# Optimization experiments

Hardware: AMD Instinct MI355X
Metric: run time of the kernel (lower is better)

Reference implementation:

```python
import jax, jax.numpy as jnp
import numpy as np

KH = KW = 5          # deformable kernel (matches offset_channels = 2*5*5)
PAD = 2              # (5-1)//2
DG = 4               # deformable groups


def conv3d(x, w, padding, bias=None):
    # x: [N,C,D,H,W], w: [O,I,kd,kh,kw]
    out = jax.lax.conv_general_dilated(
        x, w, window_strides=(1, 1, 1), padding=padding,
        dimension_numbers=('NCDHW', 'OIDHW', 'NCDHW'))
    if bias is not None:
        out = out + bias[None, :, None, None, None]
    return out


def deform_conv2d(x, offset, weight, pad=PAD, dg=DG):
    """torchvision/mmcv-style deformable conv, stride 1, groups=1, no bias.
    x: [N,C,H,W]; offset: [N, dg*2*K, H, W] ordered (group, k, (dy,dx));
    weight: [Cout, C, KH, KW]."""
    N, C, H, W = x.shape
    K = KH * KW
    off = offset.reshape(N, dg, K, 2, H, W)
    ky, kx = jnp.meshgrid(jnp.arange(KH), jnp.arange(KW), indexing='ij')
    ky = ky.reshape(K).astype(x.dtype)
    kx = kx.reshape(K).astype(x.dtype)
    # absolute sampling positions: [N,dg,K,H,W]
    base_y = ky[:, None, None] - pad + jnp.arange(H, dtype=x.dtype)[None, :, None]
    base_x = kx[:, None, None] - pad + jnp.arange(W, dtype=x.dtype)[None, None, :]
    sy = base_y[None, None] + off[:, :, :, 0]
    sx = base_x[None, None] + off[:, :, :, 1]
    y0 = jnp.floor(sy)
    x0 = jnp.floor(sx)
    wy = sy - y0
    wx = sx - x0
    y0i = y0.astype(jnp.int32)
    x0i = x0.astype(jnp.int32)
    Cg = C // dg
    xg = x.reshape(N, dg, Cg, H * W)

    def gather(yi, xi):
        valid = (yi >= 0) & (yi < H) & (xi >= 0) & (xi < W)
        yc = jnp.clip(yi, 0, H - 1)
        xc = jnp.clip(xi, 0, W - 1)
        idx = (yc * W + xc).reshape(N, dg, 1, K * H * W)
        v = jnp.take_along_axis(xg, idx, axis=3).reshape(N, dg, Cg, K, H, W)
        return v * valid[:, :, None].astype(x.dtype)

    v00 = gather(y0i, x0i)
    v01 = gather(y0i, x0i + 1)
    v10 = gather(y0i + 1, x0i)
    v11 = gather(y0i + 1, x0i + 1)
    wy_ = wy[:, :, None]
    wx_ = wx[:, :, None]
    samp = (v00 * (1 - wy_) * (1 - wx_) + v01 * (1 - wy_) * wx_
            + v10 * wy_ * (1 - wx_) + v11 * wy_ * wx_)
    samp = samp.reshape(N, C, K, H, W)             # deform groups only affect offsets
    wmat = weight.reshape(weight.shape[0], C, K)
    return jnp.einsum('nckhw,ock->nohw', samp, wmat)


def setup_inputs() -> dict:
    key = jax.random.key(0)
    k0, k1, k2, k3, k4 = jax.random.split(key, 5)
    bs, C, T, H, W = 1, 256, 4, 48, 48
    x = jax.random.normal(k0, (bs, C, T, H, W), dtype=jnp.float32)
    # spatio_offset: Conv3d(C -> dg*2*K, kernel (1,5,5), pad (0,2,2), no bias)
    w_off = jax.random.normal(k1, (DG * 2 * KH * KW, C, 1, KH, KW), dtype=jnp.float32) * 0.01
    # spatio_adaption: DeformConv2d weight, init std=0.01 (per init_weights)
    w_def = jax.random.normal(k2, (C, C, KH, KW), dtype=jnp.float32) * 0.01
    # temporal: Conv3d(C -> C, kernel (3,3,3), pad (1,1,1), with bias)
    fan_in = C * 27
    w_temp = jax.random.normal(k3, (C, C, 3, 3, 3), dtype=jnp.float32) * (1.0 / np.sqrt(fan_in))
    b_temp = jax.random.normal(k4, (C,), dtype=jnp.float32) * 0.01
    return {'x': x, 'w_off': w_off, 'w_def': w_def, 'w_temp': w_temp, 'b_temp': b_temp}


def reference(x, w_off, w_def, w_temp, b_temp):
    bs, C, T, H, W = x.shape
    # offset branch uses detached input (torch: x.detach())
    offset = conv3d(jax.lax.stop_gradient(x), w_off, [(0, 0), (PAD, PAD), (PAD, PAD)])
    off_fold = offset.transpose(0, 2, 1, 3, 4).reshape(bs * T, -1, H, W)
    x_fold = x.transpose(0, 2, 1, 3, 4).reshape(bs * T, C, H, W)
    x_spatio_fold = deform_conv2d(x_fold, off_fold, w_def)
    x_spatio = x_spatio_fold.reshape(bs, T, C, H, W).transpose(0, 2, 1, 3, 4)
    # cascaded=False branch: temporal conv on original x, then residual sum
    x_temporal = conv3d(x, w_temp, [(1, 1), (1, 1), (1, 1)], b_temp)
    return x_spatio + x_temporal
```

## Files before the change

### kernel.cpp

```cpp
#include <hip/hip_runtime.h>
#include <hip/hip_bf16.h>

#define T    4
#define C    256
#define H    48
#define W    48
#define HW   2304
#define OFFC 200
#define CK5  6400
#define CK9  2304
#define NFULL 9216
#define BPAD 72

typedef __attribute__((ext_vector_type(8))) short bf16x8;
typedef __attribute__((ext_vector_type(4))) float f32x4;

__device__ __forceinline__ unsigned short f2bf(float f) {
    unsigned int u = __float_as_uint(f);
    return (unsigned short)((u + 0x7FFFu + ((u >> 16) & 1u)) >> 16);
}
__device__ __forceinline__ float bflo(unsigned int v) { return __uint_as_float(v << 16); }
__device__ __forceinline__ float bfhi(unsigned int v) { return __uint_as_float(v & 0xFFFF0000u); }
__device__ __forceinline__ unsigned int pack2(float lo, float hi) {
    __hip_bfloat162 h = __float22bfloat162_rn(make_float2(lo, hi));
    return *reinterpret_cast<unsigned int*>(&h);
}
__device__ __forceinline__ void gload16(const void* g, void* l) {
    __builtin_amdgcn_global_load_lds(
        (const __attribute__((address_space(1))) unsigned int*)g,
        (__attribute__((address_space(3))) unsigned int*)l, 16, 0, 0);
}

__global__ __launch_bounds__(256) void prep_xt_k(const float* __restrict__ x,
                                                 const float* __restrict__ w_off,
                                                 const float* __restrict__ w_def,
                                                 const float* __restrict__ w_temp,
                                                 const float* __restrict__ bias,
                                                 unsigned short* __restrict__ wbo,
                                                 unsigned short* __restrict__ wbd,
                                                 unsigned short* __restrict__ wbT,
                                                 float* __restrict__ offb,
                                                 float* __restrict__ out,
                                                 unsigned short* __restrict__ xt) {
    __shared__ float tile[64][65];
    if (blockIdx.x >= 24320) {
        const int zb = blockIdx.x - 24320;
        const int p0 = (zb % 36) * 64, c0 = ((zb / 36) & 3) * 64, t = zb / 144;
        const int px = threadIdx.x & 63, sub = threadIdx.x >> 6;
        for (int cl = sub; cl < 64; cl += 4)
            tile[px][cl] = x[((long)(c0 + cl) * T + t) * HW + p0 + px];
        __syncthreads();
        const int seg = sub * 16;
        unsigned int pk[8];
        #pragma unroll
        for (int d = 0; d < 8; ++d)
            pk[d] = pack2(tile[px][seg + d * 2], tile[px][seg + d * 2 + 1]);
        unsigned short* orow = xt + ((long)t * HW + p0 + px) * 256 + c0 + seg;
        *(uint4*)(orow + 0) = make_uint4(pk[0], pk[1], pk[2], pk[3]);
        *(uint4*)(orow + 8) = make_uint4(pk[4], pk[5], pk[6], pk[7]);
        return;
    }
    long i = (long)blockIdx.x * 256 + threadIdx.x;
    if (i < 1638400) {
        const int c = (int)(i & 255); const int rest = (int)(i >> 8);
        const int q = rest % 25, o = rest / 25;
        wbo[(long)o * CK5 + q * 256 + c] =
            (o < OFFC) ? f2bf(w_off[((long)o * 256 + c) * 25 + q]) : (unsigned short)0;
    } else if (i < 3276800) {
        i -= 1638400;
        const int c = (int)(i & 255); const int rest = (int)(i >> 8);
        const int q = rest % 25, o = rest / 25;
        wbd[(long)o * CK5 + q * 256 + c] = f2bf(w_def[((long)o * 256 + c) * 25 + q]);
    } else if (i < 5046272) {
        i -= 3276800;
        const int c = (int)(i & 255); const int rest = (int)(i >> 8);
        const int j = rest % 9, oo = rest / 9;
        const int o = oo & 255, kt = oo >> 8;
        wbT[(long)kt * (256 * CK9) + (long)o * CK9 + j * 256 + c] =
            f2bf(w_temp[((long)o * 256 + c) * 27 + kt * 9 + j]);
    } else if (i < 5636096) {
        i -= 5046272;
        ((float4*)offb)[i] = make_float4(0.f, 0.f, 0.f, 0.f);
    } else {
        i -= 5636096;
        const float b = bias[(int)(i / 2304)];
        ((float4*)out)[i] = make_float4(b, b, b, b);
    }
}

__device__ __forceinline__ void mfma_iter(const unsigned short* __restrict__ Asl,
                                          const unsigned short* __restrict__ Bsl,
                                          int wave, int quad, int l16, f32x4 acc[4][2]) {
    const int wm = (wave & 1) * 64, wn = (wave >> 1) * 32;
    #pragma unroll
    for (int kh = 0; kh < 2; ++kh) {
        bf16x8 af[4], bfr[2];
        #pragma unroll
        for (int i = 0; i < 4; ++i) {
            const int row = wm + i * 16 + l16;
            const int slot = (kh * 4 + quad + (l16 & 7)) & 7;
            af[i] = *(const bf16x8*)(Asl + row * 64 + slot * 8);
        }
        #pragma unroll
        for (int j = 0; j < 2; ++j)
            bfr[j] = *(const bf16x8*)(Bsl + (wn + j * 16 + l16) * BPAD + kh * 32 + quad * 8);
        #pragma unroll
        for (int i = 0; i < 4; ++i)
            #pragma unroll
            for (int j = 0; j < 2; ++j)
                acc[i][j] = __builtin_amdgcn_mfma_f32_16x16x32_bf16(af[i], bfr[j], acc[i][j], 0, 0, 0);
    }
}
__device__ __forceinline__ void epilogue_atomic(float* __restrict__ Cf, int m0, int n0,
                                                int wave, int quad, int l16,
                                                int Mvalid, f32x4 acc[4][2]) {
    const int wm = (wave & 1) * 64, wn = (wave >> 1) * 32;
    #pragma unroll
    for (int i = 0; i < 4; ++i)
        #pragma unroll
        for (int rr = 0; rr < 4; ++rr) {
            const int o = m0 + wm + i * 16 + quad * 4 + rr;
            if (o >= Mvalid) continue;
            #pragma unroll
            for (int j = 0; j < 2; ++j)
                unsafeAtomicAdd(Cf + (long)o * NFULL + n0 + wn + j * 16 + l16, acc[i][j][rr]);
        }
}

__device__ __forceinline__ void gemm_shift_body(unsigned short* __restrict__ Asl,
                                                unsigned short* __restrict__ Bsl,
                                                const unsigned short* __restrict__ A, long ldA,
                                                const unsigned short* __restrict__ xt, int tsrc,
                                                float* __restrict__ Cf, int Mvalid,
                                                int m0, int n0, int k0, int iters, int mode) {
    const int tid = threadIdx.x;
    const int wave = tid >> 6, lane = tid & 63;
    const int quad = lane >> 4, l16 = lane & 15;
    const int t = n0 / HW, p0 = n0 - t * HW;
    const int px = tid >> 2, seg = tid & 3;
    const int p = p0 + px, h = p / 48, w = p - h * 48;
    const unsigned short* xts = xt + (long)tsrc * HW * 256 + seg * 8;

    const int r8 = lane >> 3, s8 = lane & 7;
    const int qg = (s8 - r8) & 7;
    const long ldAb = ldA * 2;
    const char* Ap = (const char*)A + (long)(m0 + wave * 32 + r8) * ldAb
                     + (long)k0 * 2 + qg * 16;
    const long rstep8 = 8 * ldAb;
    unsigned short* la = Asl + wave * 2048;

    auto produce = [&](int kk, uint4& v0, uint4& v1) {
        const int q = kk >> 8, cb = kk & 255;
        int qy, qx;
        if (mode == 0) { const int d = q / 5; qy = d - 2; qx = q - d * 5 - 2; }
        else           { const int d = q / 3; qy = d - 1; qx = q - d * 3 - 1; }
        const int y = h + qy, xx = w + qx;
        v0 = make_uint4(0u, 0u, 0u, 0u); v1 = v0;
        if ((y >= 0) & (y < 48) & (xx >= 0) & (xx < 48)) {
            const unsigned short* bp = xts + (y * 48 + xx) * 256 + cb;
            v0 = *(const uint4*)bp; v1 = *(const uint4*)(bp + 32);
        }
    };

    uint4 cv0, cv1;
    produce(k0, cv0, cv1);

    f32x4 acc[4][2] = {};
    for (int i = 0; i < iters; ++i) {
        __syncthreads();
        #pragma unroll
        for (int c2 = 0; c2 < 4; ++c2) gload16(Ap + c2 * rstep8, la + c2 * 512);
        Ap += 128;
        *(uint4*)(Bsl + px * BPAD + seg * 8)      = cv0;
        *(uint4*)(Bsl + px * BPAD + 32 + seg * 8) = cv1;
        __syncthreads();
        if (i + 1 < iters) produce(k0 + (i + 1) * 64, cv0, cv1);
        mfma_iter(Asl, Bsl, wave, quad, l16, acc);
    }
    epilogue_atomic(Cf, m0, n0, wave, quad, l16, Mvalid, acc);
}

__global__ __launch_bounds__(256, 4) void gemm_ot_k(const unsigned short* __restrict__ wbo,
                                                    const unsigned short* __restrict__ wbT,
                                                    const unsigned short* __restrict__ xt,
                                                    float* __restrict__ offb,
                                                    float* __restrict__ out) {
    __shared__ unsigned short Asl[128 * 64];
    __shared__ unsigned short Bsl[64 * BPAD];
    const int z = blockIdx.z, n0 = blockIdx.x * 64, m0 = blockIdx.y * 128;
    const int t = n0 / HW;
    if (z < 4) {
        gemm_shift_body(Asl, Bsl, wbo, CK5, xt, t, offb, OFFC, m0, n0, z * 1600, 25, 0);
    } else {
        const int zz = z - 4, kt = zz >> 1, half = zz & 1;
        const int tsrc = t + kt - 1;
        if (tsrc < 0 || tsrc >= T) return;
        gemm_shift_body(Asl, Bsl, wbT + (long)kt * 256 * CK9, CK9, xt, tsrc, out, C,
                        m0, n0, half * 1152, 18, 1);
    }
}

__device__ __forceinline__ void pos_calc(int h, int w, int q, float dy, float dx,
                                         float wgt[4], int idx[4]) {
    const int d = q / 5;
    const int qy = d - 2, qx = q - d * 5 - 2;
    const float sy = (float)(h + qy) + dy;
    const float sx = (float)(w + qx) + dx;
    const float y0f = floorf(sy), x0f = floorf(sx);
    const float wy = sy - y0f, wx = sx - x0f;
    const int y0 = (int)y0f, x0 = (int)x0f;
    const int y1 = y0 + 1, x1 = x0 + 1;
    float w00 = (1.f - wy) * (1.f - wx);
    float w01 = (1.f - wy) * wx;
    float w10 = wy * (1.f - wx);
    float w11 = wy * wx;
    const bool vy0 = (y0 >= 0) & (y0 < 48), vy1 = (y1 >= 0) & (y1 < 48);
    const bool vx0 = (x0 >= 0) & (x0 < 48), vx1 = (x1 >= 0) & (x1 < 48);
    if (!(vy0 & vx0)) w00 = 0.f;
    if (!(vy0 & vx1)) w01 = 0.f;
    if (!(vy1 & vx0)) w10 = 0.f;
    if (!(vy1 & vx1)) w11 = 0.f;
    const int yc0 = min(max(y0, 0), 47), yc1 = min(max(y1, 0), 47);
    const int xc0 = min(max(x0, 0), 47), xc1 = min(max(x1, 0), 47);
    wgt[0] = w00; wgt[1] = w01; wgt[2] = w10; wgt[3] = w11;
    idx[0] = yc0 * 48 + xc0; idx[1] = yc0 * 48 + xc1;
    idx[2] = yc1 * 48 + xc0; idx[3] = yc1 * 48 + xc1;
}
__device__ __forceinline__ uint4 blend4(const uint4 u[4], const float wgt[4]) {
    unsigned int pk[4];
    #pragma unroll
    for (int qi = 0; qi < 4; ++qi) {
        const unsigned int a = ((const unsigned int*)&u[0])[qi];
        const unsigned int b = ((const unsigned int*)&u[1])[qi];
        const unsigned int c = ((const unsigned int*)&u[2])[qi];
        const unsigned int d = ((const unsigned int*)&u[3])[qi];
        const float rl = wgt[0] * bflo(a) + wgt[1] * bflo(b) + wgt[2] * bflo(c) + wgt[3] * bflo(d);
        const float rh = wgt[0] * bfhi(a) + wgt[1] * bfhi(b) + wgt[2] * bfhi(c) + wgt[3] * bfhi(d);
        pk[qi] = pack2(rl, rh);
    }
    return make_uint4(pk[0], pk[1], pk[2], pk[3]);
}

__global__ __launch_bounds__(256, 4) void gemm_def_k(const unsigned short* __restrict__ A,
                                                     const unsigned short* __restrict__ xt,
                                                     const float* __restrict__ offb,
                                                     float* __restrict__ Cf) {
    __shared__ unsigned short Asl[128 * 64];
    __shared__ unsigned short Bsl[64 * BPAD];
    const int tid = threadIdx.x;
    const int wave = tid >> 6, lane = tid & 63;
    const int quad = lane >> 4, l16 = lane & 15;
    const int n0 = blockIdx.x * 64, m0 = blockIdx.y * 128, k0 = blockIdx.z * 1280;
    const int t = n0 / HW, p0 = n0 - t * HW;
    const int px = tid >> 2, seg = tid & 3;
    const int p = p0 + px, h = p / 48, w = p - h * 48;
    const int nabs = n0 + px;
    const unsigned short* xts = xt + (long)t * HW * 256 + seg * 8;

    const int r8 = lane >> 3, s8 = lane & 7;
    const int qg = (s8 - r8) & 7;
    const long ldAb = (long)CK5 * 2;
    const char* Ap = (const char*)A + (long)(m0 + wave * 32 + r8) * ldAb
                     + (long)k0 * 2 + qg * 16;
    const long rstep8 = 8 * ldAb;
    unsigned short* la = Asl + wave * 2048;

    auto off_load = [&](int kk, float& dy, float& dx) {
        const int q = kk >> 8, g = (kk & 255) >> 6;
        dy = offb[(long)(g * 50 + 2 * q) * NFULL + nabs];
        dx = offb[(long)(g * 50 + 2 * q + 1) * NFULL + nabs];
    };
    auto corners = [&](int kk, float dy, float dx, uint4 u[8], float wgt[4]) {
        const int cb = kk & 255;
        int idx[4];
        pos_calc(h, w, kk >> 8, dy, dx, wgt, idx);
        #pragma unroll
        for (int cn = 0; cn < 4; ++cn) {
            const unsigned short* bp = xts + idx[cn] * 256 + cb;
            u[cn]     = *(const uint4*)bp;
            u[cn + 4] = *(const uint4*)(bp + 32);
        }
    };

    uint4 pkv0, pkv1;
    float dyN, dxN;
    {
        float dy0, dx0;
        off_load(k0, dy0, dx0);
        uint4 u[8]; float wg[4];
        corners(k0, dy0, dx0, u, wg);
        pkv0 = blend4(u, wg);
        pkv1 = blend4(u + 4, wg);
        off_load(k0 + 64, dyN, dxN);
    }

    f32x4 acc[4][2] = {};
    for (int i = 0; i < 20; ++i) {
        const int kk = k0 + i * 64;
        __syncthreads();
        #pragma unroll
        for (int c2 = 0; c2 < 4; ++c2) gload16(Ap + c2 * rstep8, la + c2 * 512);
        Ap += 128;
        *(uint4*)(Bsl + px * BPAD + seg * 8)      = pkv0;
        *(uint4*)(Bsl + px * BPAD + 32 + seg * 8) = pkv1;
        __syncthreads();
        const bool more = (i + 1 < 20);
        uint4 u[8]; float wg[4];
        if (more) {
            corners(kk + 64, dyN, dxN, u, wg);
            if (i + 2 < 20) off_load(kk + 128, dyN, dxN);
        }
        mfma_iter(Asl, Bsl, wave, quad, l16, acc);
        if (more) {
            pkv0 = blend4(u, wg);
            pkv1 = blend4(u + 4, wg);
        }
    }
    epilogue_atomic(Cf, m0, n0, wave, quad, l16, C, acc);
}

extern "C" void kernel_launch(void* const* d_in, const int* in_sizes, int n_in,
                              void* d_out, int out_size, void* d_ws, size_t ws_size,
                              hipStream_t stream) {
    const float* x      = (const float*)d_in[0];
    const float* w_off  = (const float*)d_in[1];
    const float* w_def  = (const float*)d_in[2];
    const float* w_temp = (const float*)d_in[3];
    const float* b_temp = (const float*)d_in[4];
    float* out = (float*)d_out;

    unsigned short* xt   = (unsigned short*)d_ws;
    float*          offb = (float*)((char*)d_ws + 4718592ul);
    unsigned short* wbo  = (unsigned short*)((char*)d_ws + 14155776ul);
    unsigned short* wbd  = (unsigned short*)((char*)d_ws + 17432576ul);
    unsigned short* wbT  = (unsigned short*)((char*)d_ws + 20709376ul);

    prep_xt_k<<<24896, 256, 0, stream>>>(x, w_off, w_def, w_temp, b_temp,
                                         wbo, wbd, wbT, offb, out, xt);
    gemm_ot_k<<<dim3(144, 2, 10), 256, 0, stream>>>(wbo, wbT, xt, offb, out);
    gemm_def_k<<<dim3(144, 2, 5), 256, 0, stream>>>(wbd, xt, offb, out);
}
```

Before: 299.1 us.

## Rebalance temporal conv taps across offset and deformable GEMM launches

The temporal conv's three depth taps were all computed in the offset-conv launch. Now the outer taps (kt=0,2) stay there and the centre tap (kt=1) runs in the deformable GEMM launch. This shrinks the first launch's grid and fills the second, balancing work between the two kernels. The centre tap never hits the time boundary, so none of its blocks exit early. It adds more atomic traffic into the output during the deformable kernel.

```diff
diff --git a/kernel.cpp b/kernel.cpp
--- a/kernel.cpp
+++ b/kernel.cpp
@@ -180,11 +180,11 @@
     epilogue_atomic(Cf, m0, n0, wave, quad, l16, Mvalid, acc);
 }
 
-__global__ __launch_bounds__(256, 4) void gemm_ot_k(const unsigned short* __restrict__ wbo,
-                                                    const unsigned short* __restrict__ wbT,
-                                                    const unsigned short* __restrict__ xt,
-                                                    float* __restrict__ offb,
-                                                    float* __restrict__ out) {
+__global__ __launch_bounds__(256, 4) void gemm_ot02_k(const unsigned short* __restrict__ wbo,
+                                                      const unsigned short* __restrict__ wbT,
+                                                      const unsigned short* __restrict__ xt,
+                                                      float* __restrict__ offb,
+                                                      float* __restrict__ out) {
     __shared__ unsigned short Asl[128 * 64];
     __shared__ unsigned short Bsl[64 * BPAD];
     const int z = blockIdx.z, n0 = blockIdx.x * 64, m0 = blockIdx.y * 128;
@@ -192,7 +192,7 @@
     if (z < 4) {
         gemm_shift_body(Asl, Bsl, wbo, CK5, xt, t, offb, OFFC, m0, n0, z * 1600, 25, 0);
     } else {
-        const int zz = z - 4, kt = zz >> 1, half = zz & 1;
+        const int zz = z - 4, kt = (zz >> 1) * 2, half = zz & 1;
         const int tsrc = t + kt - 1;
         if (tsrc < 0 || tsrc >= T) return;
         gemm_shift_body(Asl, Bsl, wbT + (long)kt * 256 * CK9, CK9, xt, tsrc, out, C,
@@ -241,16 +241,16 @@
     return make_uint4(pk[0], pk[1], pk[2], pk[3]);
 }
 
-__global__ __launch_bounds__(256, 4) void gemm_def_k(const unsigned short* __restrict__ A,
-                                                     const unsigned short* __restrict__ xt,
-                                                     const float* __restrict__ offb,
-                                                     float* __restrict__ Cf) {
-    __shared__ unsigned short Asl[128 * 64];
-    __shared__ unsigned short Bsl[64 * BPAD];
+__device__ __forceinline__ void gemm_def_body(unsigned short* __restrict__ Asl,
+                                              unsigned short* __restrict__ Bsl,
+                                              const unsigned short* __restrict__ A,
+                                              const unsigned short* __restrict__ xt,
+                                              const float* __restrict__ offb,
+                                              float* __restrict__ Cf,
+                                              int m0, int n0, int k0) {
     const int tid = threadIdx.x;
     const int wave = tid >> 6, lane = tid & 63;
     const int quad = lane >> 4, l16 = lane & 15;
-    const int n0 = blockIdx.x * 64, m0 = blockIdx.y * 128, k0 = blockIdx.z * 1280;
     const int t = n0 / HW, p0 = n0 - t * HW;
     const int px = tid >> 2, seg = tid & 3;
     const int p = p0 + px, h = p / 48, w = p - h * 48;
@@ -319,6 +319,33 @@
     epilogue_atomic(Cf, m0, n0, wave, quad, l16, C, acc);
 }
 
+__device__ __forceinline__ void gemm_temp_body(unsigned short* __restrict__ Asl,
+                                               unsigned short* __restrict__ Bsl,
+                                               const unsigned short* __restrict__ A,
+                                               const unsigned short* __restrict__ xt, int tsrc,
+                                               float* __restrict__ Cf,
+                                               int m0, int n0, int k0) {
+    gemm_shift_body(Asl, Bsl, A, CK9, xt, tsrc, Cf, C, m0, n0, k0, 18, 1);
+}
+
+__global__ __launch_bounds__(256, 4) void gemm_dt1_k(const unsigned short* __restrict__ wbd,
+                                                     const unsigned short* __restrict__ wbT,
+                                                     const unsigned short* __restrict__ xt,
+                                                     const float* __restrict__ offb,
+                                                     float* __restrict__ out) {
+    __shared__ unsigned short Asl[128 * 64];
+    __shared__ unsigned short Bsl[64 * BPAD];
+    const int z = blockIdx.z, n0 = blockIdx.x * 64, m0 = blockIdx.y * 128;
+    if (z < 5) {
+        gemm_def_body(Asl, Bsl, wbd, xt, offb, out, m0, n0, z * 1280);
+    } else {
+        const int half = z - 5;
+        const int t = n0 / HW;
+        gemm_temp_body(Asl, Bsl, wbT + (long)1 * 256 * CK9, xt, t, out,
+                       m0, n0, half * 1152);
+    }
+}
+
 extern "C" void kernel_launch(void* const* d_in, const int* in_sizes, int n_in,
                               void* d_out, int out_size, void* d_ws, size_t ws_size,
                               hipStream_t stream) {
@@ -337,6 +364,6 @@
 
     prep_xt_k<<<24896, 256, 0, stream>>>(x, w_off, w_def, w_temp, b_temp,
                                          wbo, wbd, wbT, offb, out, xt);
-    gemm_ot_k<<<dim3(144, 2, 10), 256, 0, stream>>>(wbo, wbT, xt, offb, out);
-    gemm_def_k<<<dim3(144, 2, 5), 256, 0, stream>>>(wbd, xt, offb, out);
-}
+    gemm_ot02_k<<<dim3(144, 2, 8), 256, 0, stream>>>(wbo, wbT, xt, offb, out);
+    gemm_dt1_k<<<dim3(144, 2, 7), 256, 0, stream>>>(wbd, wbT, xt, offb, out);
+}
```

After: 297.4 us. About the same (-0.6%).
